# Optimization experiments

Hardware: AMD Instinct MI355X
Metric: run time of the kernel (lower is better)

Reference implementation:

```python
import jax, jax.numpy as jnp
import numpy as np

N = 100000   # nodes
E = 1600000  # edges
G = 1024     # graphs
V = 51       # attr_dims[0]+1 embedding rows (padding_idx=0)
EMB = 32
H = 2        # heads
D = 64       # hidden_dim (per-head out channels)
DC = H * D   # 128 = dim_conv
NEG_GAT = 0.2   # PyG GATConv default negative_slope
NEG_ACT = 0.05  # module's leaky_relu slope
LN_EPS = 1e-5


def setup_inputs() -> dict:
    key = jax.random.key(0)
    ks = jax.random.split(key, 20)
    def nrm(k, shape, scale=0.1):
        return jax.random.normal(k, shape, dtype=jnp.float32) * scale
    x = jax.random.randint(ks[0], (N, 1), 0, V)
    edge_index = jax.random.randint(ks[1], (2, E), 0, N)
    batch_idx = jnp.sort(jax.random.randint(ks[2], (N,), 0, G))
    return {
        'x': x, 'edge_index': edge_index, 'batch_idx': batch_idx,
        'emb': nrm(ks[3], (V, EMB)).at[0].set(0.0),  # padding_idx=0
        'ln_g': jnp.ones((EMB,), jnp.float32), 'ln_b': jnp.zeros((EMB,), jnp.float32),
        'W1': nrm(ks[4], (EMB, DC)), 'a_src1': nrm(ks[5], (H, D)), 'a_dst1': nrm(ks[6], (H, D)), 'b1': nrm(ks[7], (DC,)),
        'W2': nrm(ks[8], (DC, DC)), 'a_src2': nrm(ks[9], (H, D)), 'a_dst2': nrm(ks[10], (H, D)), 'b2': nrm(ks[11], (DC,)),
        'gw1': nrm(ks[12], (DC, D)), 'gb1': nrm(ks[13], (D,)),
        'gw2': nrm(ks[14], (D, 1)), 'gb2': nrm(ks[15], (1,)),
    }


def _gat_conv(xf, src, dst, W, a_src, a_dst, b):
    # xf: [N, in]; returns [N, H*D]. PyG GATConv, eval mode (attn dropout off).
    xw = (xf @ W).reshape(N, H, D)                           # [N,H,D]
    al_s = jnp.einsum('nhd,hd->nh', xw, a_src)
    al_d = jnp.einsum('nhd,hd->nh', xw, a_dst)
    e = jax.nn.leaky_relu(al_s[src] + al_d[dst], NEG_GAT)    # [E',H]
    m = jax.ops.segment_max(e, dst, num_segments=N)
    ex = jnp.exp(e - m[dst])
    s = jax.ops.segment_sum(ex, dst, num_segments=N)
    alpha = ex / s[dst]                                      # segment softmax over incoming edges
    msg = xw[src] * alpha[:, :, None]                        # [E',H,D]
    out = jax.ops.segment_sum(msg, dst, num_segments=N)      # [N,H,D]
    return out.reshape(N, DC) + b


def reference(x, edge_index, batch_idx, emb, ln_g, ln_b,
              W1, a_src1, a_dst1, b1, W2, a_src2, a_dst2, b2,
              gw1, gb1, gw2, gb2):
    # embedding + LayerNorm (dropout off in eval)
    xe = emb[x[:, 0]]                                        # [N,32]
    mu = jnp.mean(xe, axis=-1, keepdims=True)
    var = jnp.var(xe, axis=-1, keepdims=True)
    xe = (xe - mu) * jax.lax.rsqrt(var + LN_EPS) * ln_g + ln_b
    # add self loops (GATConv add_self_loops=True)
    ar = jnp.arange(N, dtype=edge_index.dtype)
    src = jnp.concatenate([edge_index[0], ar])
    dst = jnp.concatenate([edge_index[1], ar])
    h = jax.nn.leaky_relu(_gat_conv(xe, src, dst, W1, a_src1, a_dst1, b1), NEG_ACT)
    h = _gat_conv(h, src, dst, W2, a_src2, a_dst2, b2)       # [N,128]
    # attentional aggregation over graphs
    gate = jax.nn.leaky_relu(h @ gw1 + gb1, NEG_ACT) @ gw2 + gb2   # [N,1]
    gm = jax.ops.segment_max(gate, batch_idx, num_segments=G)
    ge = jnp.exp(gate - gm[batch_idx])
    gs = jax.ops.segment_sum(ge, batch_idx, num_segments=G)
    w = ge / gs[batch_idx]
    z = jax.ops.segment_sum(w * h, batch_idx, num_segments=G)      # [G,128]
    return h, z
```

## Files before the change

kernel.cpp:

```cpp
#include <hip/hip_runtime.h>
#include <hip/hip_bf16.h>
#include <stdint.h>

typedef unsigned short u16;
typedef unsigned int   u32;
typedef __attribute__((ext_vector_type(8))) short bf16x8;
typedef __attribute__((ext_vector_type(4))) float f32x4;

#define NEG_GAT 0.2f
#define NEG_ACT 0.05f
#define LN_EPS  1e-5f
#define NPARAM  15

__device__ __forceinline__ float bf2f(u32 bits16){
  union { u32 u; float f; } v; v.u = bits16 << 16; return v.f;
}
__device__ __forceinline__ u16 f2bf(float f){
  union { float f; u32 u; } v; v.f = f;
  u32 u = v.u;
  u32 r = (u + 0x7fffu + ((u >> 16) & 1u)) >> 16;
  return (u16)r;
}
__device__ __forceinline__ float lrelu(float x, float s){ return fmaxf(x, s * x); }

// ... 93 lines not shown
  if (gid < n) rowptr[gid] = sd[tid] - v;
  if (tid == 1023) bsums[blockIdx.x] = sd[1023];
}

__global__ void k_scanB(const int* __restrict__ bsums, int* __restrict__ boffs, int nb)
{
  __shared__ int sd[128];
  int tid = threadIdx.x;
  int v = (tid < nb) ? bsums[tid] : 0;
  sd[tid] = v;
  __syncthreads();
  for (int off = 1; off < 128; off <<= 1){
    int t = 0;
    if (tid >= off) t = sd[tid - off];
    __syncthreads();
    if (tid >= off) sd[tid] += t;
    __syncthreads();
  }
  if (tid < nb) boffs[tid] = sd[tid] - v;
}

__global__ void k_scanC(int* __restrict__ rowptr, const int* __restrict__ boffs,
                        int* __restrict__ cursor, int n, int Etot)
{
  int gid = blockIdx.x * 1024 + threadIdx.x;
  if (gid < n){
    int v = rowptr[gid] + boffs[blockIdx.x];
    rowptr[gid] = v;
    cursor[gid] = v;
  }
  if (gid == 0) rowptr[n] = Etot;
}

__global__ void k_scatter(const int* __restrict__ ei, const int* __restrict__ iflag,
                          int* __restrict__ cursor, int* __restrict__ csr, int E, int n)
{
  int e = blockIdx.x * 256 + threadIdx.x;
  if (e < E){
    int enc = *iflag;
    int s = geti(ei, e, enc);
    int d = geti(ei, E + e, enc);
    d = min(max(d, 0), n - 1);
    int pos = atomicAdd(&cursor[d], 1);
    csr[pos] = s;
  }
}

__global__ void k_check_rows(const int* __restrict__ rowptr, const int* __restrict__ cursor,
                             int n, int* __restrict__ errflag)
{
  int i = blockIdx.x * 256 + threadIdx.x;
  if (i < n){
    if (cursor[i] != rowptr[i + 1]) atomicOr(errflag, 1);
    if (i == 0 && rowptr[0] != 0)   atomicOr(errflag, 4);
  }
}

__global__ void k_check_csr(const int* __restrict__ csr, int E, int n, int* __restrict__ errflag)
{
  int e = blockIdx.x * 256 + threadIdx.x;
  if (e < E && (unsigned)csr[e] >= (unsigned)n) atomicOr(errflag, 2);
}


#define BSH   9
#define BSZ   512
#define BMSK  511
#define MAXB  2048
#define BINB  8192
#define BTH   512

__global__ void k_bhist(const int* __restrict__ ei, const int* __restrict__ iflag,
                        int* __restrict__ bcnt, int E, int N, int nbuck)
{
  __shared__ int h[MAXB];
  const int t = threadIdx.x;
  for (int i = t; i < nbuck; i += 256) h[i] = 0;
  __syncthreads();
  const int enc = *iflag;
  for (int e = blockIdx.x * 256 + t; e < E; e += gridDim.x * 256){
    int d = geti(ei, E + e, enc);
    d = min(max(d, 0), N - 1);
    atomicAdd(&h[d >> BSH], 1);
  }
  __syncthreads();
  for (int i = t; i < nbuck; i += 256){
    int c = h[i];
    if (c) atomicAdd(&bcnt[i], c);
  }
}

__global__ void k_bscan(const int* __restrict__ bcnt, int* __restrict__ boff,
                        int* __restrict__ gcur, int* __restrict__ rowptr,
                        int nbuck, int N, int E)
{
  __shared__ int sd[MAXB];
  const int lane = threadIdx.x;
  for (int i = lane; i < nbuck; i += 64) sd[i] = bcnt[i];
  __syncthreads();
  const int L = (nbuck + 63) >> 6;
  const int b0 = lane * L;
  int sum = 0;
  for (int j = 0; j < L; j++){ int idx = b0 + j; if (idx < nbuck) sum += sd[idx]; }
  int excl = sum;
  for (int off = 1; off < 64; off <<= 1){
    int x = __shfl_up(excl, off);
    if (lane >= off) excl += x;
  }
  excl -= sum;
  int run = excl;
  for (int j = 0; j < L; j++){
    int idx = b0 + j;
    if (idx < nbuck){ boff[idx] = run; gcur[idx] = run; run += sd[idx]; }
  }
  if (lane == 0){ boff[nbuck] = E; rowptr[N] = E; }
}

__global__ __launch_bounds__(BTH) void k_bbin(
    const int* __restrict__ ei, const int* __restrict__ iflag,
    int* __restrict__ gcur, u32* __restrict__ binned,
    int E, int N, int nbuck)
{
  __shared__ u32 stage[BINB];
  __shared__ u16 sbk[BINB];
  __shared__ int hist[MAXB];
  __shared__ int base[MAXB];
  __shared__ int gpos[MAXB];
  const int t   = threadIdx.x;
  const int e0  = blockIdx.x * BINB;
  const int cnt = min(BINB, E - e0);
  const int enc = *iflag;

  for (int i = t; i < nbuck; i += BTH) hist[i] = 0;
  __syncthreads();

  u32 pv[16]; int bk[16]; int rk[16];
  #pragma unroll
  for (int k = 0; k < 16; k++){
    bk[k] = -1;
    int lo = k * BTH + t;
    if (lo < cnt){
      int e = e0 + lo;
      int s = geti(ei, e, enc);
      int d = geti(ei, E + e, enc);
      s = min(max(s, 0), N - 1);
      d = min(max(d, 0), N - 1);
      int b = d >> BSH;
      pv[k] = ((u32)s << BSH) | (u32)(d & BMSK);
      bk[k] = b;
      rk[k] = atomicAdd(&hist[b], 1);
    }
  }
  __syncthreads();

  if (t < 64){
    const int L = (nbuck + 63) >> 6;
    const int b0 = t * L;
    int sum = 0;
    for (int j = 0; j < L; j++){ int idx = b0 + j; if (idx < nbuck) sum += hist[idx]; }
    int excl = sum;
    for (int off = 1; off < 64; off <<= 1){
      int x = __shfl_up(excl, off);
      if (t >= off) excl += x;
    }
    excl -= sum;
    int run = excl;
    for (int j = 0; j < L; j++){
      int idx = b0 + j;
      if (idx < nbuck){ base[idx] = run; run += hist[idx]; }
    }
  }
  __syncthreads();

  for (int i = t; i < nbuck; i += BTH){
    int c = hist[i];
    gpos[i] = c ? atomicAdd(&gcur[i], c) : 0;
  }
  __syncthreads();

  #pragma unroll
  for (int k = 0; k < 16; k++){
    if (bk[k] >= 0){
      int slot = base[bk[k]] + rk[k];
      stage[slot] = pv[k];
      sbk[slot]   = (u16)bk[k];
    }
  }
  __syncthreads();

  for (int j = t; j < cnt; j += BTH){
    int b = sbk[j];
    binned[gpos[b] + (j - base[b])] = stage[j];
  }
}

__global__ __launch_bounds__(256) void k_bcsr(
    const u32* __restrict__ binned, const int* __restrict__ boff,
    int* __restrict__ rowptr, int* __restrict__ csr, int N, int nbuck)
{
  __shared__ int cnt[BSZ];
  __shared__ int rp[BSZ];
  __shared__ int cur[BSZ];
  const int b = blockIdx.x;
  const int t = threadIdx.x;
  const int lo = boff[b], hi = boff[b + 1];

  for (int i = t; i < BSZ; i += 256){ cnt[i] = 0; cur[i] = 0; }
  __syncthreads();

  for (int j = lo + t; j < hi; j += 256)
    atomicAdd(&cnt[binned[j] & BMSK], 1);
  __syncthreads();

  if (t < 64){
    const int b0 = t * 8;
    int sum = 0;
    #pragma unroll
    for (int j = 0; j < 8; j++) sum += cnt[b0 + j];
    int excl = sum;
    for (int off = 1; off < 64; off <<= 1){
      int x = __shfl_up(excl, off);
      if (t >= off) excl += x;
    }
    excl -= sum;
    int run = excl;
    #pragma unroll
    for (int j = 0; j < 8; j++){ rp[b0 + j] = run; run += cnt[b0 + j]; }
  }
  __syncthreads();

  const int node0 = b << BSH;
  for (int i = t; i < BSZ; i += 256){
    int node = node0 + i;
    if (node < N) rowptr[node] = lo + rp[i];
  }

  for (int j = lo + t; j < hi; j += 256){
    u32 pvv = binned[j];
    int dl  = pvv & BMSK;
    int pos = lo + rp[dl] + atomicAdd(&cur[dl], 1);
    csr[pos] = (int)(pvv >> BSH);
  }
}


__global__ void k_stamp_if(const int* __restrict__ errflag, float* __restrict__ out, int nel)
{
  int f = *errflag;
  if (f == 0) return;
  float s = 500.0f + 100.0f * (float)f;
  int i = blockIdx.x * 256 + threadIdx.x;
  if (i < nel) out[i] = s;
}

__global__ void k_stamp(float* __restrict__ out, int nel, float val)
{
  int i = blockIdx.x * 256 + threadIdx.x;
  if (i < nel) out[i] = val;
}


__global__ void k_prep(const float* __restrict__ emb,
                       const float* __restrict__ ln_g, const float* __restrict__ ln_b,
                       const float* __restrict__ W1, const float* __restrict__ a_src,
                       const float* __restrict__ a_dst,
                       u16* __restrict__ xwv, float* __restrict__ alsv, float* __restrict__ aldv)
{
  __shared__ float se[32];
  __shared__ float stats[2];
  __shared__ float sxw[128];
  const int v = blockIdx.x, t = threadIdx.x;
  if (t < 32) se[t] = emb[v * 32 + t];
  __syncthreads();
  if (t == 0){
    float s1 = 0.f, s2 = 0.f;
    for (int k = 0; k < 32; k++){ s1 += se[k]; s2 += se[k] * se[k]; }
    float mu = s1 * (1.f / 32.f);
    float var = s2 * (1.f / 32.f) - mu * mu;
    stats[0] = mu; stats[1] = rsqrtf(var + LN_EPS);
  }
  __syncthreads();
  const float mu = stats[0], rs = stats[1];
  float o = 0.f;
  for (int k = 0; k < 32; k++){
    float xe = (se[k] - mu) * rs * ln_g[k] + ln_b[k];
    o += xe * W1[k * 128 + t];
  }
  sxw[t] = o;
  xwv[v * 128 + t] = f2bf(o);
  __syncthreads();
  if (t < 2){
    float ps = 0.f, pd = 0.f;
    for (int d = 0; d < 64; d++){
      float vv = sxw[t * 64 + d];
      ps += vv * a_src[t * 64 + d];
      pd += vv * a_dst[t * 64 + d];
    }
    alsv[2 * v + t] = ps;
    aldv[2 * v + t] = pd;
  }
}


__global__ __launch_bounds__(64, 8) void k_gatw1(
    const int* __restrict__ rowptr, const int* __restrict__ csr,
    const int* __restrict__ x, const int* __restrict__ iflag,
    const float* __restrict__ alsv, const float* __restrict__ aldv,
    const u16* __restrict__ xwv, const float* __restrict__ bias,
    int V, float* __restrict__ out)
{
  const int i    = blockIdx.x;
  const int lane = threadIdx.x;
  const int sub  = lane >> 4;
  const int c16  = lane & 15;
  const int enc  = *iflag;
  const int r0 = rowptr[i], deg = rowptr[i + 1] - r0, total = deg + 1;
  int vi = geti(x, i, enc); vi = min(max(vi, 0), V - 1);
  const float ad0 = aldv[2 * vi], ad1 = aldv[2 * vi + 1];

  float sum0 = 0.f, sum1 = 0.f;
  float acc[8];
  #pragma unroll
  for (int r = 0; r < 8; r++) acc[r] = 0.f;

  if (total <= 64){
    int vs = vi;
    float a0 = -3.0e38f, a1 = -3.0e38f;
    if (lane < total){
      int s = (lane < deg) ? csr[r0 + lane] : i;
      int v = geti(x, s, enc);
      vs = min(max(v, 0), V - 1);
      float2 as = *(const float2*)(alsv + 2 * vs);
      a0 = lrelu(as.x + ad0, NEG_GAT);
      a1 = lrelu(as.y + ad1, NEG_GAT);
    }
    float m0 = a0, m1 = a1;
    #pragma unroll
    for (int off = 32; off; off >>= 1){
      m0 = fmaxf(m0, __shfl_xor(m0, off));
      m1 = fmaxf(m1, __shfl_xor(m1, off));
    }
    float ex0 = 0.f, ex1 = 0.f;
    if (lane < total){ ex0 = __expf(a0 - m0); ex1 = __expf(a1 - m1); }
    sum0 = ex0; sum1 = ex1;
    int qmax = (total + 3) & ~3;
    for (int q = 0; q < qmax; q += 4){
      int   j  = q + sub;
      int   vj = __shfl(vs, j);
      float e0 = __shfl(ex0, j);
      float e1 = __shfl(ex1, j);
      float ej = (c16 < 8) ? e0 : e1;
      uint4 w = *(const uint4*)(xwv + (size_t)vj * 128 + c16 * 8);
      acc[0] += ej * bf2f(w.x & 0xffffu); acc[1] += ej * bf2f(w.x >> 16);
      acc[2] += ej * bf2f(w.y & 0xffffu); acc[3] += ej * bf2f(w.y >> 16);
      acc[4] += ej * bf2f(w.z & 0xffffu); acc[5] += ej * bf2f(w.z >> 16);
      acc[6] += ej * bf2f(w.w & 0xffffu); acc[7] += ej * bf2f(w.w >> 16);
    }
  } else {
    float m0 = -3.0e38f, m1 = -3.0e38f;
    for (int k = lane; k < total; k += 64){
      int s = (k < deg) ? csr[r0 + k] : i;
      int v = geti(x, s, enc); v = min(max(v, 0), V - 1);
      float2 as = *(const float2*)(alsv + 2 * v);
      m0 = fmaxf(m0, lrelu(as.x + ad0, NEG_GAT));
      m1 = fmaxf(m1, lrelu(as.y + ad1, NEG_GAT));
    }
    #pragma unroll
    for (int off = 32; off; off >>= 1){
      m0 = fmaxf(m0, __shfl_xor(m0, off));
      m1 = fmaxf(m1, __shfl_xor(m1, off));
    }
    for (int base = 0; base < total; base += 64){
      int k = base + lane;
      int vs = vi; float ex0 = 0.f, ex1 = 0.f;
      if (k < total){
        int s = (k < deg) ? csr[r0 + k] : i;
        int v = geti(x, s, enc); vs = min(max(v, 0), V - 1);
        float2 as = *(const float2*)(alsv + 2 * vs);
        ex0 = __expf(lrelu(as.x + ad0, NEG_GAT) - m0);
        ex1 = __expf(lrelu(as.y + ad1, NEG_GAT) - m1);
      }
      sum0 += ex0; sum1 += ex1;
      int cnt = min(64, total - base);
      int qmax = (cnt + 3) & ~3;
      for (int q = 0; q < qmax; q += 4){
        int   j  = q + sub;
        int   vj = __shfl(vs, j);
        float e0 = __shfl(ex0, j);
        float e1 = __shfl(ex1, j);
        float ej = (c16 < 8) ? e0 : e1;
        uint4 w = *(const uint4*)(xwv + (size_t)vj * 128 + c16 * 8);
        acc[0] += ej * bf2f(w.x & 0xffffu); acc[1] += ej * bf2f(w.x >> 16);
        acc[2] += ej * bf2f(w.y & 0xffffu); acc[3] += ej * bf2f(w.y >> 16);
        acc[4] += ej * bf2f(w.z & 0xffffu); acc[5] += ej * bf2f(w.z >> 16);
        acc[6] += ej * bf2f(w.w & 0xffffu); acc[7] += ej * bf2f(w.w >> 16);
      }
    }
  }

  #pragma unroll
  for (int off = 32; off; off >>= 1){
    sum0 += __shfl_xor(sum0, off);
    sum1 += __shfl_xor(sum1, off);
  }
  #pragma unroll
  for (int r = 0; r < 8; r++){
    acc[r] += __shfl_xor(acc[r], 16);
    acc[r] += __shfl_xor(acc[r], 32);
  }

  if (sub == 0){
    float inv = 1.f / ((c16 < 8) ? sum0 : sum1);
    const float4* bp = (const float4*)(bias + c16 * 8);
    float4 b0 = bp[0], b1 = bp[1];
    float4 o0, o1;
    o0.x = lrelu(acc[0] * inv + b0.x, NEG_ACT); o0.y = lrelu(acc[1] * inv + b0.y, NEG_ACT);
    o0.z = lrelu(acc[2] * inv + b0.z, NEG_ACT); o0.w = lrelu(acc[3] * inv + b0.w, NEG_ACT);
    o1.x = lrelu(acc[4] * inv + b1.x, NEG_ACT); o1.y = lrelu(acc[5] * inv + b1.y, NEG_ACT);
    o1.z = lrelu(acc[6] * inv + b1.z, NEG_ACT); o1.w = lrelu(acc[7] * inv + b1.w, NEG_ACT);
    float* op = out + (size_t)i * 128 + c16 * 8;
    *(float4*)op       = o0;
    *(float4*)(op + 4) = o1;
  }
}


__global__ __launch_bounds__(64, 8) void k_gatw2(
    const int* __restrict__ rowptr, const int* __restrict__ csr,
    const float* __restrict__ al_s, const float* __restrict__ al_d,
    const u16* __restrict__ xw, const float* __restrict__ bias,
    int apply_act, float* __restrict__ out)
{
  const int i    = blockIdx.x;
  const int lane = threadIdx.x;
  const int sub  = lane >> 4;
  const int c16  = lane & 15;
  const int r0 = rowptr[i], deg = rowptr[i + 1] - r0, total = deg + 1;
  const float2 ad = *(const float2*)(al_d + 2 * i);

  float sum0 = 0.f, sum1 = 0.f;
  float acc[8];
  #pragma unroll
  for (int r = 0; r < 8; r++) acc[r] = 0.f;

  if (total <= 64){
    int s = i;
    float a0 = -3.0e38f, a1 = -3.0e38f;
    if (lane < total){
      s = (lane < deg) ? csr[r0 + lane] : i;
      float2 as = *(const float2*)(al_s + 2 * s);
      a0 = lrelu(as.x + ad.x, NEG_GAT);
      a1 = lrelu(as.y + ad.y, NEG_GAT);
    }
    float m0 = a0, m1 = a1;
    #pragma unroll
    for (int off = 32; off; off >>= 1){
      m0 = fmaxf(m0, __shfl_xor(m0, off));
      m1 = fmaxf(m1, __shfl_xor(m1, off));
    }
    float ex0 = 0.f, ex1 = 0.f;
    if (lane < total){ ex0 = __expf(a0 - m0); ex1 = __expf(a1 - m1); }
    sum0 = ex0; sum1 = ex1;
    int qmax = (total + 3) & ~3;
    for (int q = 0; q < qmax; q += 4){
      int   j  = q + sub;
      int   sj = __shfl(s, j);
      float e0 = __shfl(ex0, j);
      float e1 = __shfl(ex1, j);
      float ej = (c16 < 8) ? e0 : e1;
      uint4 w = *(const uint4*)(xw + (size_t)sj * 128 + c16 * 8);
      acc[0] += ej * bf2f(w.x & 0xffffu); acc[1] += ej * bf2f(w.x >> 16);
      acc[2] += ej * bf2f(w.y & 0xffffu); acc[3] += ej * bf2f(w.y >> 16);
      acc[4] += ej * bf2f(w.z & 0xffffu); acc[5] += ej * bf2f(w.z >> 16);
      acc[6] += ej * bf2f(w.w & 0xffffu); acc[7] += ej * bf2f(w.w >> 16);
    }
  } else {
    float m0 = -3.0e38f, m1 = -3.0e38f;
    for (int k = lane; k < total; k += 64){
      int s = (k < deg) ? csr[r0 + k] : i;
      float2 as = *(const float2*)(al_s + 2 * s);
      m0 = fmaxf(m0, lrelu(as.x + ad.x, NEG_GAT));
      m1 = fmaxf(m1, lrelu(as.y + ad.y, NEG_GAT));
    }
    #pragma unroll
    for (int off = 32; off; off >>= 1){
      m0 = fmaxf(m0, __shfl_xor(m0, off));
      m1 = fmaxf(m1, __shfl_xor(m1, off));
    }
    for (int base = 0; base < total; base += 64){
      int k = base + lane;
      int s = i; float ex0 = 0.f, ex1 = 0.f;
      if (k < total){
        s = (k < deg) ? csr[r0 + k] : i;
        float2 as = *(const float2*)(al_s + 2 * s);
        ex0 = __expf(lrelu(as.x + ad.x, NEG_GAT) - m0);
        ex1 = __expf(lrelu(as.y + ad.y, NEG_GAT) - m1);
      }
      sum0 += ex0; sum1 += ex1;
      int cnt = min(64, total - base);
      int qmax = (cnt + 3) & ~3;
      for (int q = 0; q < qmax; q += 4){
        int   j  = q + sub;
        int   sj = __shfl(s, j);
        float e0 = __shfl(ex0, j);
        float e1 = __shfl(ex1, j);
        float ej = (c16 < 8) ? e0 : e1;
        uint4 w = *(const uint4*)(xw + (size_t)sj * 128 + c16 * 8);
        acc[0] += ej * bf2f(w.x & 0xffffu); acc[1] += ej * bf2f(w.x >> 16);
        acc[2] += ej * bf2f(w.y & 0xffffu); acc[3] += ej * bf2f(w.y >> 16);
        acc[4] += ej * bf2f(w.z & 0xffffu); acc[5] += ej * bf2f(w.z >> 16);
        acc[6] += ej * bf2f(w.w & 0xffffu); acc[7] += ej * bf2f(w.w >> 16);
      }
    }
  }

  #pragma unroll
  for (int off = 32; off; off >>= 1){
    sum0 += __shfl_xor(sum0, off);
    sum1 += __shfl_xor(sum1, off);
  }
  #pragma unroll
  for (int r = 0; r < 8; r++){
    acc[r] += __shfl_xor(acc[r], 16);
    acc[r] += __shfl_xor(acc[r], 32);
  }

  if (sub == 0){
    float inv = 1.f / ((c16 < 8) ? sum0 : sum1);
    const float4* bp = (const float4*)(bias + c16 * 8);
    float4 b0 = bp[0], b1 = bp[1];
    float4 o0, o1;
    o0.x = acc[0] * inv + b0.x; o0.y = acc[1] * inv + b0.y;
    o0.z = acc[2] * inv + b0.z; o0.w = acc[3] * inv + b0.w;
    o1.x = acc[4] * inv + b1.x; o1.y = acc[5] * inv + b1.y;
    o1.z = acc[6] * inv + b1.z; o1.w = acc[7] * inv + b1.w;
    if (apply_act){
      o0.x = lrelu(o0.x, NEG_ACT); o0.y = lrelu(o0.y, NEG_ACT);
      o0.z = lrelu(o0.z, NEG_ACT); o0.w = lrelu(o0.w, NEG_ACT);
      o1.x = lrelu(o1.x, NEG_ACT); o1.y = lrelu(o1.y, NEG_ACT);
      o1.z = lrelu(o1.z, NEG_ACT); o1.w = lrelu(o1.w, NEG_ACT);
    }
    float* op = out + (size_t)i * 128 + c16 * 8;
    *(float4*)op       = o0;
    *(float4*)(op + 4) = o1;
  }
}


__global__ void k_packW(const float* __restrict__ W, int ncols, int ntiles,
                        u16* __restrict__ pb)
{
  const int ktile = blockIdx.x / ntiles;
  const int ntile = blockIdx.x % ntiles;
  const int lane  = threadIdx.x;
  const int n  = ntile * 16 + (lane & 15);
  const int k0 = ktile * 32 + (lane >> 4) * 8;
  u16* dst = pb + ((size_t)blockIdx.x * 64 + lane) * 8;
  #pragma unroll
  for (int j = 0; j < 8; j++)
    dst[j] = f2bf(W[(k0 + j) * ncols + n]);
}


__global__ __launch_bounds__(256, 2) void k_node2m(
    const float* __restrict__ h1, const u16* __restrict__ pb2,
    const float* __restrict__ a_src, const float* __restrict__ a_dst,
    int N, u16* __restrict__ xw, float* __restrict__ al_s, float* __restrict__ al_d)
{
  const int wave = threadIdx.x >> 6;
  const int lane = threadIdx.x & 63;
  const int rowbase = blockIdx.x * 64 + wave * 16;
  const int m    = lane & 15;
  const int quad = lane >> 4;

  int arow = rowbase + m; if (arow >= N) arow = N - 1;
  const float* aptr = h1 + (size_t)arow * 128 + quad * 8;

  f32x4 acc[8];
  #pragma unroll
  for (int nt = 0; nt < 8; nt++) acc[nt] = (f32x4){0.f, 0.f, 0.f, 0.f};

  #pragma unroll
  for (int kt = 0; kt < 4; kt++){
    float4 a0 = *(const float4*)(aptr + kt * 32);
    float4 a1 = *(const float4*)(aptr + kt * 32 + 4);
    bf16x8 af;
    af[0] = (short)f2bf(a0.x); af[1] = (short)f2bf(a0.y);
    af[2] = (short)f2bf(a0.z); af[3] = (short)f2bf(a0.w);
    af[4] = (short)f2bf(a1.x); af[5] = (short)f2bf(a1.y);
    af[6] = (short)f2bf(a1.z); af[7] = (short)f2bf(a1.w);
    const u16* bbase = pb2 + (((size_t)kt * 8) * 64 + lane) * 8;
    #pragma unroll
    for (int nt = 0; nt < 8; nt++){
      bf16x8 bf = *(const bf16x8*)(bbase + (size_t)nt * 64 * 8);
      acc[nt] = __builtin_amdgcn_mfma_f32_16x16x32_bf16(af, bf, acc[nt], 0, 0, 0);
    }
  }

  float asv[8], adv[8];
  #pragma unroll
  for (int nt = 0; nt < 8; nt++){
    asv[nt] = a_src[nt * 16 + m];
    adv[nt] = a_dst[nt * 16 + m];
  }
  #pragma unroll
  for (int r = 0; r < 4; r++){
    int row = rowbase + quad * 4 + r;
    bool ok = row < N;
    float s0 = 0.f, s1 = 0.f, d0 = 0.f, d1 = 0.f;
    #pragma unroll
    for (int nt = 0; nt < 8; nt++){
      float v = acc[nt][r];
      if (ok) xw[(size_t)row * 128 + nt * 16 + m] = f2bf(v);
      if (nt < 4){ s0 += v * asv[nt]; d0 += v * adv[nt]; }
      else       { s1 += v * asv[nt]; d1 += v * adv[nt]; }
    }
    #pragma unroll
    for (int off = 1; off < 16; off <<= 1){
      s0 += __shfl_xor(s0, off); s1 += __shfl_xor(s1, off);
      d0 += __shfl_xor(d0, off); d1 += __shfl_xor(d1, off);
    }
    if (ok && m == 0){
      al_s[2 * row] = s0; al_s[2 * row + 1] = s1;
      al_d[2 * row] = d0; al_d[2 * row + 1] = d1;
    }
  }
}


__global__ __launch_bounds__(256, 2) void k_gatem(
    const float* __restrict__ h, const u16* __restrict__ pbg,
    const float* __restrict__ gb1, const float* __restrict__ gw2,
    const float* __restrict__ gb2, int N, float* __restrict__ gate)
{
  const int wave = threadIdx.x >> 6;
  const int lane = threadIdx.x & 63;
  const int rowbase = blockIdx.x * 64 + wave * 16;
  const int m    = lane & 15;
  const int quad = lane >> 4;

  int arow = rowbase + m; if (arow >= N) arow = N - 1;
  const float* aptr = h + (size_t)arow * 128 + quad * 8;

  f32x4 acc[4];
  #pragma unroll
  for (int nt = 0; nt < 4; nt++) acc[nt] = (f32x4){0.f, 0.f, 0.f, 0.f};

  #pragma unroll
  for (int kt = 0; kt < 4; kt++){
    float4 a0 = *(const float4*)(aptr + kt * 32);
    float4 a1 = *(const float4*)(aptr + kt * 32 + 4);
    bf16x8 af;
    af[0] = (short)f2bf(a0.x); af[1] = (short)f2bf(a0.y);
    af[2] = (short)f2bf(a0.z); af[3] = (short)f2bf(a0.w);
    af[4] = (short)f2bf(a1.x); af[5] = (short)f2bf(a1.y);
    af[6] = (short)f2bf(a1.z); af[7] = (short)f2bf(a1.w);
    const u16* bbase = pbg + (((size_t)kt * 4) * 64 + lane) * 8;
    #pragma unroll
    for (int nt = 0; nt < 4; nt++){
      bf16x8 bf = *(const bf16x8*)(bbase + (size_t)nt * 64 * 8);
      acc[nt] = __builtin_amdgcn_mfma_f32_16x16x32_bf16(af, bf, acc[nt], 0, 0, 0);
    }
  }

  float gbv[4], g2v[4];
  #pragma unroll
  for (int nt = 0; nt < 4; nt++){
    gbv[nt] = gb1[nt * 16 + m];
    g2v[nt] = gw2[nt * 16 + m];
  }
  const float g2b = gb2[0];
  #pragma unroll
  for (int r = 0; r < 4; r++){
    int row = rowbase + quad * 4 + r;
    float q = 0.f;
    #pragma unroll
    for (int nt = 0; nt < 4; nt++)
      q += lrelu(acc[nt][r] + gbv[nt], NEG_ACT) * g2v[nt];
    #pragma unroll
    for (int off = 1; off < 16; off <<= 1) q += __shfl_xor(q, off);
    if (row < N && m == 0) gate[row] = q + g2b;
  }
}


__global__ void k_graphsw(const int* __restrict__ batch, const int* __restrict__ iflag,
                          const float* __restrict__ gate,
                          const float* __restrict__ h, float* __restrict__ zout, int N)
{
  __shared__ int   range[2];
  __shared__ float red[4];
  const int g = blockIdx.x, t = threadIdx.x;
  const int wave = t >> 6;
  if (t == 0){
    const int enc = *iflag;
    int lo = 0, hi = N;
    while (lo < hi){ int mid = (lo + hi) >> 1; if (geti(batch, mid, enc) < g) lo = mid + 1; else hi = mid; }
    range[0] = lo;
    hi = N;
    while (lo < hi){ int mid = (lo + hi) >> 1; if (geti(batch, mid, enc) < g + 1) lo = mid + 1; else hi = mid; }
    range[1] = lo;
  }
  __syncthreads();
  const int st = range[0], en = range[1];

  float m = -3.0e38f;
  for (int k = st + t; k < en; k += 128) m = fmaxf(m, gate[k]);
  #pragma unroll
  for (int off = 32; off; off >>= 1) m = fmaxf(m, __shfl_xor(m, off));
  if ((t & 63) == 0) red[wave] = m;
  __syncthreads();
  m = fmaxf(red[0], red[1]);

  float s = 0.f;
  for (int k = st + t; k < en; k += 128) s += __expf(gate[k] - m);
  #pragma unroll
  for (int off = 32; off; off >>= 1) s += __shfl_xor(s, off);
  if ((t & 63) == 0) red[2 + wave] = s;
  __syncthreads();
  s = red[2] + red[3];

  float z = 0.f;
  const float inv = 1.f / s;
  for (int k = st; k < en; k++){
    float wk = __expf(gate[k] - m) * inv;
    z += wk * h[(size_t)k * 128 + t];
  }
  zout[(size_t)g * 128 + t] = z;
}


extern "C" void kernel_launch(void* const* d_in, const int* in_sizes, int n_in,
                              void* d_out, int out_size, void* d_ws, size_t ws_size,
                              hipStream_t stream)
{
  const int* x      = (const int*)d_in[0];
  const int* ei     = (const int*)d_in[1];
  const int* batch  = (const int*)d_in[2];

  const int N = in_sizes[0];
  const int E = in_sizes[1] / 2;
  const int V = in_sizes[3] / 32;
  const int G = out_size / 128 - N;

  char* p = (char*)d_ws;
  auto alloc = [&](size_t bytes) -> char* {
    char* r = p; p += (bytes + 255) & ~(size_t)255; return r;
  };
  int*   multi  = (int*)  alloc((size_t)N * 4);
  int*   rowptr = (int*)  alloc((size_t)(N + 1) * 4);
  int*   csr    = (int*)  alloc((size_t)E * 4);
  int*   bsums  = (int*)  alloc(4096);
  int*   boffs  = (int*)  alloc(4096);
  int*   flags  = (int*)  alloc(256);
  int*   fflag  = flags;
  int*   iflag  = flags + 1;
  int*   errflg = flags + 2;
  float* al_s   = (float*)alloc((size_t)N * 2 * 4);
  float* al_d   = (float*)alloc((size_t)N * 2 * 4);
  u16*   xw     = (u16*)  alloc((size_t)N * 128 * 2);
  u16*   xwv    = (u16*)  alloc((size_t)V * 128 * 2);
  float* alsv   = (float*)alloc((size_t)V * 2 * 4);
  float* aldv   = (float*)alloc((size_t)V * 2 * 4);
  u16*   pb2    = (u16*)  alloc((size_t)128 * 128 * 2);
  u16*   pbg    = (u16*)  alloc((size_t)128 * 64 * 2);

  const int nbuck = (N + BSZ - 1) >> BSH;
  int*   bcnt   = (int*)  alloc((size_t)(MAXB) * 4);
  int*   boff   = (int*)  alloc((size_t)(MAXB + 1) * 4);
  int*   gcur   = (int*)  alloc((size_t)(MAXB) * 4);
  u32*   binned = (u32*)  alloc((size_t)E * 4);

  CvtParams cp;
  float* fpar[NPARAM];
  int maxn = 0;
  for (int pi = 0; pi < NPARAM; pi++){
    int n = in_sizes[3 + pi];
    fpar[pi] = (float*)alloc((size_t)n * 4);
    cp.src[pi] = d_in[3 + pi];
    cp.dst[pi] = fpar[pi];
    cp.n[pi]   = n;
    if (n > maxn) maxn = n;
  }
  const size_t needed = (size_t)(p - (char*)d_ws);

  const float* emb    = fpar[0];
  const float* ln_g   = fpar[1];
  const float* ln_b   = fpar[2];
  const float* W1     = fpar[3];
  const float* a_src1 = fpar[4];
  const float* a_dst1 = fpar[5];
  const float* b1     = fpar[6];
  const float* W2     = fpar[7];
  const float* a_src2 = fpar[8];
  const float* a_dst2 = fpar[9];
  const float* b2     = fpar[10];
  const float* gw1    = fpar[11];
  const float* gb1    = fpar[12];
  const float* gw2    = fpar[13];
  const float* gb2    = fpar[14];
  (void)n_in;

  int ob = (out_size + 255) / 256;
  if (ws_size < needed){
    k_stamp<<<ob, 256, 0, stream>>>((float*)d_out, out_size, 9999.0f);
    return;
  }

  int*   counts = multi;
  int*   cursor = multi;
  float* gate   = (float*)multi;
  float* hbuf   = (float*)d_out;
  float* zbuf   = (float*)d_out + (size_t)N * 128;

  k_detect<<<1, 64, 0, stream>>>((const u32*)d_in[4], ei, fflag, iflag, errflg);
  dim3 cgrid((maxn + 255) / 256, NPARAM);
  k_convert<<<cgrid, 256, 0, stream>>>(cp, fflag);

  int eb = (E + 255) / 256;
  int nb = (N + 1023) / 1024;
  int nb256 = (N + 255) / 256;

  k_check_sorted<<<nb256, 256, 0, stream>>>(batch, iflag, N, errflg);
  k_check_x<<<nb256, 256, 0, stream>>>(x, iflag, N, V, errflg);
  k_check_edges<<<eb, 256, 0, stream>>>(ei, iflag, E, N, errflg);

  if (nbuck <= MAXB){
    hipMemsetAsync(bcnt, 0, (size_t)nbuck * 4, stream);
    k_bhist<<<256, 256, 0, stream>>>(ei, iflag, bcnt, E, N, nbuck);
    k_bscan<<<1, 64, 0, stream>>>(bcnt, boff, gcur, rowptr, nbuck, N, E);
    k_bbin<<<(E + BINB - 1) / BINB, BTH, 0, stream>>>(ei, iflag, gcur, binned, E, N, nbuck);
    k_bcsr<<<nbuck, 256, 0, stream>>>(binned, boff, rowptr, csr, N, nbuck);
  } else {
    hipMemsetAsync(counts, 0, (size_t)N * 4, stream);
    hipMemsetAsync(csr, 0xFF, (size_t)E * 4, stream);
    k_hist<<<eb, 256, 0, stream>>>(ei, iflag, counts, E, N);
    k_scanA<<<nb, 1024, 0, stream>>>(counts, rowptr, bsums, N);
    k_scanB<<<1, 128, 0, stream>>>(bsums, boffs, nb);
    k_scanC<<<nb, 1024, 0, stream>>>(rowptr, boffs, cursor, N, E);
    k_scatter<<<eb, 256, 0, stream>>>(ei, iflag, cursor, csr, E, N);
    k_check_rows<<<nb256, 256, 0, stream>>>(rowptr, cursor, N, errflg);
    k_check_csr<<<eb, 256, 0, stream>>>(csr, E, N, errflg);
  }

  k_packW<<<32, 64, 0, stream>>>(W2, 128, 8, pb2);
  k_packW<<<16, 64, 0, stream>>>(gw1, 64, 4, pbg);

  k_prep<<<V, 128, 0, stream>>>(emb, ln_g, ln_b, W1, a_src1, a_dst1, xwv, alsv, aldv);
  k_gatw1<<<N, 64, 0, stream>>>(rowptr, csr, x, iflag, alsv, aldv, xwv, b1, V, hbuf);

  const int gblk = (N + 63) / 64;
  k_node2m<<<gblk, 256, 0, stream>>>(hbuf, pb2, a_src2, a_dst2, N, xw, al_s, al_d);

  k_gatw2<<<N, 64, 0, stream>>>(rowptr, csr, al_s, al_d, xw, b2, 0, hbuf);

  k_gatem<<<gblk, 256, 0, stream>>>(hbuf, pbg, gb1, gw2, gb2, N, gate);
  k_graphsw<<<G, 128, 0, stream>>>(batch, iflag, gate, hbuf, zbuf, N);

  k_stamp_if<<<ob, 256, 0, stream>>>(errflg, (float*)d_out, out_size);
}
```

Measured before the change: 398.4 us.

## Stage vocab table in LDS, persist GAT kernels, prefetch gathers, split graph pooling

Layer-1 GAT now copies the small per-vocab projected table and attention scores into shared memory. Each block runs four waves in a grid-stride loop over nodes, so neighbour gathers read LDS instead of global memory. Layer-2 GAT gets the same persistent 4-wave layout, passes edge metadata through LDS instead of shuffles, and software-prefetches the next gathered row. Graph pooling uses 256 threads with two halves splitting the node range, at the cost of one extra reduction step and a fallback kernel when the vocab table is too large for LDS.

Result: faster. 381.5 us (-4.2%).

```diff
diff --git a/kernel.cpp b/kernel.cpp
--- a/kernel.cpp
+++ b/kernel.cpp
@@ -419,7 +419,149 @@
 }
 
 
-__global__ __launch_bounds__(64, 8) void k_gatw1(
+__global__ __launch_bounds__(256, 4) void k_gatw1(
+    const int* __restrict__ rowptr, const int* __restrict__ csr,
+    const int* __restrict__ x, const int* __restrict__ iflag,
+    const float* __restrict__ alsv, const float* __restrict__ aldv,
+    const u16* __restrict__ xwv, const float* __restrict__ bias,
+    int N, int V, float* __restrict__ out)
+{
+  extern __shared__ char smem[];
+  u16*    sxwv  = (u16*)smem;
+  float2* sals  = (float2*)(smem + (size_t)V * 256);
+  float2* sald  = sals + V;
+  float4* sedge = (float4*)(smem + (size_t)V * 256 + (size_t)V * 16);
+
+  const int tid = threadIdx.x;
+  const int enc = *iflag;
+
+  {
+    const uint4* gx = (const uint4*)xwv;
+    uint4* lx = (uint4*)sxwv;
+    for (int idx = tid; idx < V * 16; idx += 256) lx[idx] = gx[idx];
+    const float2* ga = (const float2*)alsv;
+    const float2* gd = (const float2*)aldv;
+    for (int idx = tid; idx < V; idx += 256){ sals[idx] = ga[idx]; sald[idx] = gd[idx]; }
+  }
+  __syncthreads();
+
+  const int wave = tid >> 6;
+  const int lane = tid & 63;
+  const int sub  = lane >> 4;
+  const int c16  = lane & 15;
+  float4* mst = sedge + wave * 64;
+
+  for (int i = blockIdx.x * 4 + wave; i < N; i += gridDim.x * 4){
+    const int r0 = rowptr[i], deg = rowptr[i + 1] - r0, total = deg + 1;
+    int vi = geti(x, i, enc); vi = min(max(vi, 0), V - 1);
+    const float2 ad = sald[vi];
+
+    float sum0 = 0.f, sum1 = 0.f;
+    float acc[8];
+    #pragma unroll
+    for (int r = 0; r < 8; r++) acc[r] = 0.f;
+
+    if (total <= 64){
+      int vs = vi;
+      float a0 = -3.0e38f, a1 = -3.0e38f;
+      if (lane < total){
+        int s = (lane < deg) ? csr[r0 + lane] : i;
+        int v = geti(x, s, enc);
+        vs = min(max(v, 0), V - 1);
+        float2 as = sals[vs];
+        a0 = lrelu(as.x + ad.x, NEG_GAT);
+        a1 = lrelu(as.y + ad.y, NEG_GAT);
+      }
+      float m0 = a0, m1 = a1;
+      #pragma unroll
+      for (int off = 32; off; off >>= 1){
+        m0 = fmaxf(m0, __shfl_xor(m0, off));
+        m1 = fmaxf(m1, __shfl_xor(m1, off));
+      }
+      float ex0 = 0.f, ex1 = 0.f;
+      if (lane < total){ ex0 = __expf(a0 - m0); ex1 = __expf(a1 - m1); }
+      sum0 = ex0; sum1 = ex1;
+      mst[lane] = make_float4(__int_as_float(vs), ex0, ex1, 0.f);
+      int qmax = (total + 3) & ~3;
+      for (int q = 0; q < qmax; q += 4){
+        float4 md = mst[q + sub];
+        int   vj = __float_as_int(md.x);
+        float ej = (c16 < 8) ? md.y : md.z;
+        uint4 w = *(const uint4*)(sxwv + vj * 128 + c16 * 8);
+        acc[0] += ej * bf2f(w.x & 0xffffu); acc[1] += ej * bf2f(w.x >> 16);
+        acc[2] += ej * bf2f(w.y & 0xffffu); acc[3] += ej * bf2f(w.y >> 16);
+        acc[4] += ej * bf2f(w.z & 0xffffu); acc[5] += ej * bf2f(w.z >> 16);
+        acc[6] += ej * bf2f(w.w & 0xffffu); acc[7] += ej * bf2f(w.w >> 16);
+      }
+    } else {
+      float m0 = -3.0e38f, m1 = -3.0e38f;
+      for (int k = lane; k < total; k += 64){
+        int s = (k < deg) ? csr[r0 + k] : i;
+        int v = geti(x, s, enc); v = min(max(v, 0), V - 1);
+        float2 as = sals[v];
+        m0 = fmaxf(m0, lrelu(as.x + ad.x, NEG_GAT));
+        m1 = fmaxf(m1, lrelu(as.y + ad.y, NEG_GAT));
+      }
+      #pragma unroll
+      for (int off = 32; off; off >>= 1){
+        m0 = fmaxf(m0, __shfl_xor(m0, off));
+        m1 = fmaxf(m1, __shfl_xor(m1, off));
+      }
+      for (int base = 0; base < total; base += 64){
+        int k = base + lane;
+        int vs = vi; float ex0 = 0.f, ex1 = 0.f;
+        if (k < total){
+          int s = (k < deg) ? csr[r0 + k] : i;
+          int v = geti(x, s, enc); vs = min(max(v, 0), V - 1);
+          float2 as = sals[vs];
+          ex0 = __expf(lrelu(as.x + ad.x, NEG_GAT) - m0);
+          ex1 = __expf(lrelu(as.y + ad.y, NEG_GAT) - m1);
+        }
+        sum0 += ex0; sum1 += ex1;
+        mst[lane] = make_float4(__int_as_float(vs), ex0, ex1, 0.f);
+        int cnt = min(64, total - base);
+        int qmax = (cnt + 3) & ~3;
+        for (int q = 0; q < qmax; q += 4){
+          float4 md = mst[q + sub];
+          int   vj = __float_as_int(md.x);
+          float ej = (c16 < 8) ? md.y : md.z;
+          uint4 w = *(const uint4*)(sxwv + vj * 128 + c16 * 8);
+          acc[0] += ej * bf2f(w.x & 0xffffu); acc[1] += ej * bf2f(w.x >> 16);
+          acc[2] += ej * bf2f(w.y & 0xffffu); acc[3] += ej * bf2f(w.y >> 16);
+          acc[4] += ej * bf2f(w.z & 0xffffu); acc[5] += ej * bf2f(w.z >> 16);
+          acc[6] += ej * bf2f(w.w & 0xffffu); acc[7] += ej * bf2f(w.w >> 16);
+        }
+      }
+    }
+
+    #pragma unroll
+    for (int off = 32; off; off >>= 1){
+      sum0 += __shfl_xor(sum0, off);
+      sum1 += __shfl_xor(sum1, off);
+    }
+    #pragma unroll
+    for (int r = 0; r < 8; r++){
+      acc[r] += __shfl_xor(acc[r], 16);
+      acc[r] += __shfl_xor(acc[r], 32);
+    }
+
+    if (sub == 0){
+      float inv = 1.f / ((c16 < 8) ? sum0 : sum1);
+      const float4* bp = (const float4*)(bias + c16 * 8);
+      float4 b0 = bp[0], b1 = bp[1];
+      float4 o0, o1;
+      o0.x = lrelu(acc[0] * inv + b0.x, NEG_ACT); o0.y = lrelu(acc[1] * inv + b0.y, NEG_ACT);
+      o0.z = lrelu(acc[2] * inv + b0.z, NEG_ACT); o0.w = lrelu(acc[3] * inv + b0.w, NEG_ACT);
+      o1.x = lrelu(acc[4] * inv + b1.x, NEG_ACT); o1.y = lrelu(acc[5] * inv + b1.y, NEG_ACT);
+      o1.z = lrelu(acc[6] * inv + b1.z, NEG_ACT); o1.w = lrelu(acc[7] * inv + b1.w, NEG_ACT);
+      float* op = out + (size_t)i * 128 + c16 * 8;
+      *(float4*)op       = o0;
+      *(float4*)(op + 4) = o1;
+    }
+  }
+}
+
+__global__ __launch_bounds__(64, 8) void k_gatw1g(
     const int* __restrict__ rowptr, const int* __restrict__ csr,
     const int* __restrict__ x, const int* __restrict__ iflag,
     const float* __restrict__ alsv, const float* __restrict__ aldv,
@@ -440,27 +582,32 @@
   #pragma unroll
   for (int r = 0; r < 8; r++) acc[r] = 0.f;
 
-  if (total <= 64){
-    int vs = vi;
-    float a0 = -3.0e38f, a1 = -3.0e38f;
-    if (lane < total){
-      int s = (lane < deg) ? csr[r0 + lane] : i;
-      int v = geti(x, s, enc);
-      vs = min(max(v, 0), V - 1);
+  float m0 = -3.0e38f, m1 = -3.0e38f;
+  for (int k = lane; k < total; k += 64){
+    int s = (k < deg) ? csr[r0 + k] : i;
+    int v = geti(x, s, enc); v = min(max(v, 0), V - 1);
+    float2 as = *(const float2*)(alsv + 2 * v);
+    m0 = fmaxf(m0, lrelu(as.x + ad0, NEG_GAT));
+    m1 = fmaxf(m1, lrelu(as.y + ad1, NEG_GAT));
+  }
+  #pragma unroll
+  for (int off = 32; off; off >>= 1){
+    m0 = fmaxf(m0, __shfl_xor(m0, off));
+    m1 = fmaxf(m1, __shfl_xor(m1, off));
+  }
+  for (int base = 0; base < total; base += 64){
+    int k = base + lane;
+    int vs = vi; float ex0 = 0.f, ex1 = 0.f;
+    if (k < total){
+      int s = (k < deg) ? csr[r0 + k] : i;
+      int v = geti(x, s, enc); vs = min(max(v, 0), V - 1);
       float2 as = *(const float2*)(alsv + 2 * vs);
-      a0 = lrelu(as.x + ad0, NEG_GAT);
-      a1 = lrelu(as.y + ad1, NEG_GAT);
-    }
-    float m0 = a0, m1 = a1;
-    #pragma unroll
-    for (int off = 32; off; off >>= 1){
-      m0 = fmaxf(m0, __shfl_xor(m0, off));
-      m1 = fmaxf(m1, __shfl_xor(m1, off));
-    }
-    float ex0 = 0.f, ex1 = 0.f;
-    if (lane < total){ ex0 = __expf(a0 - m0); ex1 = __expf(a1 - m1); }
-    sum0 = ex0; sum1 = ex1;
-    int qmax = (total + 3) & ~3;
+      ex0 = __expf(lrelu(as.x + ad0, NEG_GAT) - m0);
+      ex1 = __expf(lrelu(as.y + ad1, NEG_GAT) - m1);
+    }
+    sum0 += ex0; sum1 += ex1;
+    int cnt = min(64, total - base);
+    int qmax = (cnt + 3) & ~3;
     for (int q = 0; q < qmax; q += 4){
       int   j  = q + sub;
       int   vj = __shfl(vs, j);
@@ -472,46 +619,6 @@
       acc[2] += ej * bf2f(w.y & 0xffffu); acc[3] += ej * bf2f(w.y >> 16);
       acc[4] += ej * bf2f(w.z & 0xffffu); acc[5] += ej * bf2f(w.z >> 16);
       acc[6] += ej * bf2f(w.w & 0xffffu); acc[7] += ej * bf2f(w.w >> 16);
-    }
-  } else {
-    float m0 = -3.0e38f, m1 = -3.0e38f;
-    for (int k = lane; k < total; k += 64){
-      int s = (k < deg) ? csr[r0 + k] : i;
-      int v = geti(x, s, enc); v = min(max(v, 0), V - 1);
-      float2 as = *(const float2*)(alsv + 2 * v);
-      m0 = fmaxf(m0, lrelu(as.x + ad0, NEG_GAT));
-      m1 = fmaxf(m1, lrelu(as.y + ad1, NEG_GAT));
-    }
-    #pragma unroll
-    for (int off = 32; off; off >>= 1){
-      m0 = fmaxf(m0, __shfl_xor(m0, off));
-      m1 = fmaxf(m1, __shfl_xor(m1, off));
-    }
-    for (int base = 0; base < total; base += 64){
-      int k = base + lane;
-      int vs = vi; float ex0 = 0.f, ex1 = 0.f;
-      if (k < total){
-        int s = (k < deg) ? csr[r0 + k] : i;
-        int v = geti(x, s, enc); vs = min(max(v, 0), V - 1);
-        float2 as = *(const float2*)(alsv + 2 * vs);
-        ex0 = __expf(lrelu(as.x + ad0, NEG_GAT) - m0);
-        ex1 = __expf(lrelu(as.y + ad1, NEG_GAT) - m1);
-      }
-      sum0 += ex0; sum1 += ex1;
-      int cnt = min(64, total - base);
-      int qmax = (cnt + 3) & ~3;
-      for (int q = 0; q < qmax; q += 4){
-        int   j  = q + sub;
-        int   vj = __shfl(vs, j);
-        float e0 = __shfl(ex0, j);
-        float e1 = __shfl(ex1, j);
-        float ej = (c16 < 8) ? e0 : e1;
-        uint4 w = *(const uint4*)(xwv + (size_t)vj * 128 + c16 * 8);
-        acc[0] += ej * bf2f(w.x & 0xffffu); acc[1] += ej * bf2f(w.x >> 16);
-        acc[2] += ej * bf2f(w.y & 0xffffu); acc[3] += ej * bf2f(w.y >> 16);
-        acc[4] += ej * bf2f(w.z & 0xffffu); acc[5] += ej * bf2f(w.z >> 16);
-        acc[6] += ej * bf2f(w.w & 0xffffu); acc[7] += ej * bf2f(w.w >> 16);
-      }
     }
   }
 
@@ -542,124 +649,131 @@
 }
 
 
-__global__ __launch_bounds__(64, 8) void k_gatw2(
+__global__ __launch_bounds__(256, 4) void k_gatw2(
     const int* __restrict__ rowptr, const int* __restrict__ csr,
     const float* __restrict__ al_s, const float* __restrict__ al_d,
     const u16* __restrict__ xw, const float* __restrict__ bias,
-    int apply_act, float* __restrict__ out)
-{
-  const int i    = blockIdx.x;
-  const int lane = threadIdx.x;
+    int apply_act, int N, float* __restrict__ out)
+{
+  __shared__ float4 sedge[4][64];
+  const int tid  = threadIdx.x;
+  const int wave = tid >> 6;
+  const int lane = tid & 63;
   const int sub  = lane >> 4;
   const int c16  = lane & 15;
-  const int r0 = rowptr[i], deg = rowptr[i + 1] - r0, total = deg + 1;
-  const float2 ad = *(const float2*)(al_d + 2 * i);
-
-  float sum0 = 0.f, sum1 = 0.f;
-  float acc[8];
-  #pragma unroll
-  for (int r = 0; r < 8; r++) acc[r] = 0.f;
-
-  if (total <= 64){
-    int s = i;
-    float a0 = -3.0e38f, a1 = -3.0e38f;
-    if (lane < total){
-      s = (lane < deg) ? csr[r0 + lane] : i;
-      float2 as = *(const float2*)(al_s + 2 * s);
-      a0 = lrelu(as.x + ad.x, NEG_GAT);
-      a1 = lrelu(as.y + ad.y, NEG_GAT);
-    }
-    float m0 = a0, m1 = a1;
+  float4* mst = sedge[wave];
+
+  for (int i = blockIdx.x * 4 + wave; i < N; i += gridDim.x * 4){
+    const int r0 = rowptr[i], deg = rowptr[i + 1] - r0, total = deg + 1;
+    const float2 ad = *(const float2*)(al_d + 2 * i);
+
+    float sum0 = 0.f, sum1 = 0.f;
+    float acc[8];
+    #pragma unroll
+    for (int r = 0; r < 8; r++) acc[r] = 0.f;
+
+    if (total <= 64){
+      int s = i;
+      float a0 = -3.0e38f, a1 = -3.0e38f;
+      if (lane < total){
+        s = (lane < deg) ? csr[r0 + lane] : i;
+        float2 as = *(const float2*)(al_s + 2 * s);
+        a0 = lrelu(as.x + ad.x, NEG_GAT);
+        a1 = lrelu(as.y + ad.y, NEG_GAT);
+      }
+      float m0 = a0, m1 = a1;
+      #pragma unroll
+      for (int off = 32; off; off >>= 1){
+        m0 = fmaxf(m0, __shfl_xor(m0, off));
+        m1 = fmaxf(m1, __shfl_xor(m1, off));
+      }
+      float ex0 = 0.f, ex1 = 0.f;
+      if (lane < total){ ex0 = __expf(a0 - m0); ex1 = __expf(a1 - m1); }
+      sum0 = ex0; sum1 = ex1;
+      mst[lane] = make_float4(__int_as_float(s), ex0, ex1, 0.f);
+      int qmax = (total + 3) & ~3;
+      float4 md = mst[sub];
+      uint4  w  = *(const uint4*)(xw + (size_t)__float_as_int(md.x) * 128 + c16 * 8);
+      for (int q = 0; q < qmax; q += 4){
+        float ej = (c16 < 8) ? md.y : md.z;
+        uint4 wc = w;
+        if (q + 4 < qmax){
+          md = mst[q + 4 + sub];
+          w  = *(const uint4*)(xw + (size_t)__float_as_int(md.x) * 128 + c16 * 8);
+        }
+        acc[0] += ej * bf2f(wc.x & 0xffffu); acc[1] += ej * bf2f(wc.x >> 16);
+        acc[2] += ej * bf2f(wc.y & 0xffffu); acc[3] += ej * bf2f(wc.y >> 16);
+        acc[4] += ej * bf2f(wc.z & 0xffffu); acc[5] += ej * bf2f(wc.z >> 16);
+        acc[6] += ej * bf2f(wc.w & 0xffffu); acc[7] += ej * bf2f(wc.w >> 16);
+      }
+    } else {
+      float m0 = -3.0e38f, m1 = -3.0e38f;
+      for (int k = lane; k < total; k += 64){
+        int s = (k < deg) ? csr[r0 + k] : i;
+        float2 as = *(const float2*)(al_s + 2 * s);
+        m0 = fmaxf(m0, lrelu(as.x + ad.x, NEG_GAT));
+        m1 = fmaxf(m1, lrelu(as.y + ad.y, NEG_GAT));
+      }
+      #pragma unroll
+      for (int off = 32; off; off >>= 1){
+        m0 = fmaxf(m0, __shfl_xor(m0, off));
+        m1 = fmaxf(m1, __shfl_xor(m1, off));
+      }
+      for (int base = 0; base < total; base += 64){
+        int k = base + lane;
+        int s = i; float ex0 = 0.f, ex1 = 0.f;
+        if (k < total){
+          s = (k < deg) ? csr[r0 + k] : i;
+          float2 as = *(const float2*)(al_s + 2 * s);
+          ex0 = __expf(lrelu(as.x + ad.x, NEG_GAT) - m0);
+          ex1 = __expf(lrelu(as.y + ad.y, NEG_GAT) - m1);
+        }
+        sum0 += ex0; sum1 += ex1;
+        mst[lane] = make_float4(__int_as_float(s), ex0, ex1, 0.f);
+        int cnt = min(64, total - base);
+        int qmax = (cnt + 3) & ~3;
+        for (int q = 0; q < qmax; q += 4){
+          float4 md = mst[q + sub];
+          float ej = (c16 < 8) ? md.y : md.z;
+          uint4 w = *(const uint4*)(xw + (size_t)__float_as_int(md.x) * 128 + c16 * 8);
+          acc[0] += ej * bf2f(w.x & 0xffffu); acc[1] += ej * bf2f(w.x >> 16);
+          acc[2] += ej * bf2f(w.y & 0xffffu); acc[3] += ej * bf2f(w.y >> 16);
+          acc[4] += ej * bf2f(w.z & 0xffffu); acc[5] += ej * bf2f(w.z >> 16);
+          acc[6] += ej * bf2f(w.w & 0xffffu); acc[7] += ej * bf2f(w.w >> 16);
+        }
+      }
+    }
+
     #pragma unroll
     for (int off = 32; off; off >>= 1){
-      m0 = fmaxf(m0, __shfl_xor(m0, off));
-      m1 = fmaxf(m1, __shfl_xor(m1, off));
-    }
-    float ex0 = 0.f, ex1 = 0.f;
-    if (lane < total){ ex0 = __expf(a0 - m0); ex1 = __expf(a1 - m1); }
-    sum0 = ex0; sum1 = ex1;
-    int qmax = (total + 3) & ~3;
-    for (int q = 0; q < qmax; q += 4){
-      int   j  = q + sub;
-      int   sj = __shfl(s, j);
-      float e0 = __shfl(ex0, j);
-      float e1 = __shfl(ex1, j);
-      float ej = (c16 < 8) ? e0 : e1;
-      uint4 w = *(const uint4*)(xw + (size_t)sj * 128 + c16 * 8);
-      acc[0] += ej * bf2f(w.x & 0xffffu); acc[1] += ej * bf2f(w.x >> 16);
-      acc[2] += ej * bf2f(w.y & 0xffffu); acc[3] += ej * bf2f(w.y >> 16);
-      acc[4] += ej * bf2f(w.z & 0xffffu); acc[5] += ej * bf2f(w.z >> 16);
-      acc[6] += ej * bf2f(w.w & 0xffffu); acc[7] += ej * bf2f(w.w >> 16);
-    }
-  } else {
-    float m0 = -3.0e38f, m1 = -3.0e38f;
-    for (int k = lane; k < total; k += 64){
-      int s = (k < deg) ? csr[r0 + k] : i;
-      float2 as = *(const float2*)(al_s + 2 * s);
-      m0 = fmaxf(m0, lrelu(as.x + ad.x, NEG_GAT));
-      m1 = fmaxf(m1, lrelu(as.y + ad.y, NEG_GAT));
-    }
-    #pragma unroll
-    for (int off = 32; off; off >>= 1){
-      m0 = fmaxf(m0, __shfl_xor(m0, off));
-      m1 = fmaxf(m1, __shfl_xor(m1, off));
-    }
-    for (int base = 0; base < total; base += 64){
-      int k = base + lane;
-      int s = i; float ex0 = 0.f, ex1 = 0.f;
-      if (k < total){
-        s = (k < deg) ? csr[r0 + k] : i;
-        float2 as = *(const float2*)(al_s + 2 * s);
-        ex0 = __expf(lrelu(as.x + ad.x, NEG_GAT) - m0);
-        ex1 = __expf(lrelu(as.y + ad.y, NEG_GAT) - m1);
-      }
-      sum0 += ex0; sum1 += ex1;
-      int cnt = min(64, total - base);
-      int qmax = (cnt + 3) & ~3;
-      for (int q = 0; q < qmax; q += 4){
-        int   j  = q + sub;
-        int   sj = __shfl(s, j);
-        float e0 = __shfl(ex0, j);
-        float e1 = __shfl(ex1, j);
-        float ej = (c16 < 8) ? e0 : e1;
-        uint4 w = *(const uint4*)(xw + (size_t)sj * 128 + c16 * 8);
-        acc[0] += ej * bf2f(w.x & 0xffffu); acc[1] += ej * bf2f(w.x >> 16);
-        acc[2] += ej * bf2f(w.y & 0xffffu); acc[3] += ej * bf2f(w.y >> 16);
-        acc[4] += ej * bf2f(w.z & 0xffffu); acc[5] += ej * bf2f(w.z >> 16);
-        acc[6] += ej * bf2f(w.w & 0xffffu); acc[7] += ej * bf2f(w.w >> 16);
-      }
-    }
-  }
-
-  #pragma unroll
-  for (int off = 32; off; off >>= 1){
-    sum0 += __shfl_xor(sum0, off);
-    sum1 += __shfl_xor(sum1, off);
-  }
-  #pragma unroll
-  for (int r = 0; r < 8; r++){
-    acc[r] += __shfl_xor(acc[r], 16);
-    acc[r] += __shfl_xor(acc[r], 32);
-  }
-
-  if (sub == 0){
-    float inv = 1.f / ((c16 < 8) ? sum0 : sum1);
-    const float4* bp = (const float4*)(bias + c16 * 8);
-    float4 b0 = bp[0], b1 = bp[1];
-    float4 o0, o1;
-    o0.x = acc[0] * inv + b0.x; o0.y = acc[1] * inv + b0.y;
-    o0.z = acc[2] * inv + b0.z; o0.w = acc[3] * inv + b0.w;
-    o1.x = acc[4] * inv + b1.x; o1.y = acc[5] * inv + b1.y;
-    o1.z = acc[6] * inv + b1.z; o1.w = acc[7] * inv + b1.w;
-    if (apply_act){
-      o0.x = lrelu(o0.x, NEG_ACT); o0.y = lrelu(o0.y, NEG_ACT);
-      o0.z = lrelu(o0.z, NEG_ACT); o0.w = lrelu(o0.w, NEG_ACT);
-      o1.x = lrelu(o1.x, NEG_ACT); o1.y = lrelu(o1.y, NEG_ACT);
-      o1.z = lrelu(o1.z, NEG_ACT); o1.w = lrelu(o1.w, NEG_ACT);
-    }
-    float* op = out + (size_t)i * 128 + c16 * 8;
-    *(float4*)op       = o0;
-    *(float4*)(op + 4) = o1;
+      sum0 += __shfl_xor(sum0, off);
+      sum1 += __shfl_xor(sum1, off);
+    }
+    #pragma unroll
+    for (int r = 0; r < 8; r++){
+      acc[r] += __shfl_xor(acc[r], 16);
+      acc[r] += __shfl_xor(acc[r], 32);
+    }
+
+    if (sub == 0){
+      float inv = 1.f / ((c16 < 8) ? sum0 : sum1);
+      const float4* bp = (const float4*)(bias + c16 * 8);
+      float4 b0 = bp[0], b1 = bp[1];
+      float4 o0, o1;
+      o0.x = acc[0] * inv + b0.x; o0.y = acc[1] * inv + b0.y;
+      o0.z = acc[2] * inv + b0.z; o0.w = acc[3] * inv + b0.w;
+      o1.x = acc[4] * inv + b1.x; o1.y = acc[5] * inv + b1.y;
+      o1.z = acc[6] * inv + b1.z; o1.w = acc[7] * inv + b1.w;
+      if (apply_act){
+        o0.x = lrelu(o0.x, NEG_ACT); o0.y = lrelu(o0.y, NEG_ACT);
+        o0.z = lrelu(o0.z, NEG_ACT); o0.w = lrelu(o0.w, NEG_ACT);
+        o1.x = lrelu(o1.x, NEG_ACT); o1.y = lrelu(o1.y, NEG_ACT);
+        o1.z = lrelu(o1.z, NEG_ACT); o1.w = lrelu(o1.w, NEG_ACT);
+      }
+      float* op = out + (size_t)i * 128 + c16 * 8;
+      *(float4*)op       = o0;
+      *(float4*)(op + 4) = o1;
+    }
   }
 }
 
@@ -801,14 +915,16 @@
 }
 
 
-__global__ void k_graphsw(const int* __restrict__ batch, const int* __restrict__ iflag,
-                          const float* __restrict__ gate,
-                          const float* __restrict__ h, float* __restrict__ zout, int N)
+__global__ __launch_bounds__(256) void k_graphsw(
+    const int* __restrict__ batch, const int* __restrict__ iflag,
+    const float* __restrict__ gate,
+    const float* __restrict__ h, float* __restrict__ zout, int N)
 {
   __shared__ int   range[2];
-  __shared__ float red[4];
+  __shared__ float red[8];
+  __shared__ float sz[128];
   const int g = blockIdx.x, t = threadIdx.x;
-  const int wave = t >> 6;
+  const int wave = t >> 6, lane = t & 63;
   if (t == 0){
     const int enc = *iflag;
     int lo = 0, hi = N;
@@ -822,28 +938,31 @@
   const int st = range[0], en = range[1];
 
   float m = -3.0e38f;
-  for (int k = st + t; k < en; k += 128) m = fmaxf(m, gate[k]);
+  for (int k = st + t; k < en; k += 256) m = fmaxf(m, gate[k]);
   #pragma unroll
   for (int off = 32; off; off >>= 1) m = fmaxf(m, __shfl_xor(m, off));
-  if ((t & 63) == 0) red[wave] = m;
-  __syncthreads();
-  m = fmaxf(red[0], red[1]);
+  if (lane == 0) red[wave] = m;
+  __syncthreads();
+  m = fmaxf(fmaxf(red[0], red[1]), fmaxf(red[2], red[3]));
 
   float s = 0.f;
-  for (int k = st + t; k < en; k += 128) s += __expf(gate[k] - m);
+  for (int k = st + t; k < en; k += 256) s += __expf(gate[k] - m);
   #pragma unroll
   for (int off = 32; off; off >>= 1) s += __shfl_xor(s, off);
-  if ((t & 63) == 0) red[2 + wave] = s;
-  __syncthreads();
-  s = red[2] + red[3];
-
+  if (lane == 0) red[4 + wave] = s;
+  __syncthreads();
+  s = (red[4] + red[5]) + (red[6] + red[7]);
+
+  const float inv = 1.f / s;
+  const int half = t >> 7, t2 = t & 127;
   float z = 0.f;
-  const float inv = 1.f / s;
-  for (int k = st; k < en; k++){
+  for (int k = st + half; k < en; k += 2){
     float wk = __expf(gate[k] - m) * inv;
-    z += wk * h[(size_t)k * 128 + t];
-  }
-  zout[(size_t)g * 128 + t] = z;
+    z += wk * h[(size_t)k * 128 + t2];
+  }
+  if (half == 1) sz[t2] = z;
+  __syncthreads();
+  if (half == 0) zout[(size_t)g * 128 + t2] = z + sz[t2];
 }
 
 
@@ -964,15 +1083,22 @@
   k_packW<<<16, 64, 0, stream>>>(gw1, 64, 4, pbg);
 
   k_prep<<<V, 128, 0, stream>>>(emb, ln_g, ln_b, W1, a_src1, a_dst1, xwv, alsv, aldv);
-  k_gatw1<<<N, 64, 0, stream>>>(rowptr, csr, x, iflag, alsv, aldv, xwv, b1, V, hbuf);
+
+  const int gwb = min(2048, (N + 3) / 4);
+  const size_t smem1 = (size_t)V * 272 + 4096;
+  if (smem1 <= 64 * 1024){
+    k_gatw1<<<gwb, 256, smem1, stream>>>(rowptr, csr, x, iflag, alsv, aldv, xwv, b1, N, V, hbuf);
+  } else {
+    k_gatw1g<<<N, 64, 0, stream>>>(rowptr, csr, x, iflag, alsv, aldv, xwv, b1, V, hbuf);
+  }
 
   const int gblk = (N + 63) / 64;
   k_node2m<<<gblk, 256, 0, stream>>>(hbuf, pb2, a_src2, a_dst2, N, xw, al_s, al_d);
 
-  k_gatw2<<<N, 64, 0, stream>>>(rowptr, csr, al_s, al_d, xw, b2, 0, hbuf);
+  k_gatw2<<<gwb, 256, 0, stream>>>(rowptr, csr, al_s, al_d, xw, b2, 0, N, hbuf);
 
   k_gatem<<<gblk, 256, 0, stream>>>(hbuf, pbg, gb1, gw2, gb2, N, gate);
-  k_graphsw<<<G, 128, 0, stream>>>(batch, iflag, gate, hbuf, zbuf, N);
+  k_graphsw<<<G, 256, 0, stream>>>(batch, iflag, gate, hbuf, zbuf, N);
 
   k_stamp_if<<<ob, 256, 0, stream>>>(errflg, (float*)d_out, out_size);
 }
```
